# Optimization experiments

Measured on AMD Instinct MI355X. Metric: run time of the kernel, lower is better.

## Reference

```python
import jax, jax.numpy as jnp
from jax import lax
import numpy as np

IMG = 1024                      # image_size (square)
RPN_TRAIN_THRES = 0.5
RATIOS = jnp.array([0.5, 1.0, 2.0], jnp.float32)
SCALES = jnp.array([0.2, 0.4, 0.7], jnp.float32)
K_GT = 16


def _conv(x, w, b, stride):
    # NHWC x HWIO -> NHWC, VALID padding (keras Conv2D default)
    return lax.conv_general_dilated(x, w, (stride, stride), 'VALID',
                                    dimension_numbers=('NHWC', 'HWIO', 'NHWC')) + b


def _anchor_set():
    # [-w/2, -h/2, w/2, h/2] for 9 ratio/scale combos
    rs = jnp.sqrt(RATIOS)[:, None]                      # (3,1)
    ws = (SCALES[None, :] * rs).reshape(-1)             # (9,)
    hs = (SCALES[None, :] / rs).reshape(-1)
    return jnp.stack([ws, hs, ws, hs], axis=1) * 0.5 * jnp.array([-1.0, -1.0, 1.0, 1.0], jnp.float32)


def _anchors_pre(h, w):
    # mirrors generate_anchors_pre (incl. tf.transpose reversing axes -> (W,H,4));
    # feature map is square here so the layout matches the original.
    x = jnp.arange(0.0, 1.0, 1.0 / w, dtype=jnp.float32)
    y = jnp.arange(0.0, 1.0, 1.0 / h, dtype=jnp.float32)
    xx, yy = jnp.meshgrid(x, y)                         # (H,W)
    centers = jnp.stack([xx, yy, xx, yy], 0).transpose(2, 1, 0)  # (W,H,4)
    return centers[:, :, None, :] + _anchor_set()       # (W,H,9,4)


def _iou(b1, b2, gw, gh):
    gwh = jnp.array([gw, gh], jnp.float32)
    s1 = jnp.prod(b1[..., 2:] - b1[..., :2] + gwh, axis=-1)
    s2 = jnp.prod(b2[..., 2:] - b2[..., :2] + gwh, axis=-1)
    xa = jnp.maximum(b1[..., 0], b2[..., 0])
    ya = jnp.maximum(b1[..., 1], b2[..., 1])
    xb = jnp.minimum(b1[..., 2], b2[..., 2])
    yb = jnp.minimum(b1[..., 3], b2[..., 3])
    inter = jnp.maximum(xb - xa + gw, 0.0) * jnp.maximum(yb - ya + gh, 0.0)
    return inter / (s1 + s2 - inter)


def setup_inputs() -> dict:
    key = jax.random.key(0)
    ks = jax.random.split(key, 10)
    image = jax.random.uniform(ks[0], (1, IMG, IMG, 3), jnp.float32)
    cxy = jax.random.uniform(ks[1], (K_GT, 2), jnp.float32, 0.2, 0.8)
    wh = jax.random.uniform(ks[2], (K_GT, 2), jnp.float32, 0.1, 0.4)
    gt_boxes = jnp.concatenate([cxy - wh / 2, cxy + wh / 2], axis=1)  # (K,4) x1,y1,x2,y2
    Wb = jax.random.normal(ks[3], (4, 4, 3, 128), jnp.float32) * 0.05
    bb = jnp.zeros((128,), jnp.float32)
    Wi = jax.random.normal(ks[4], (3, 3, 128, 256), jnp.float32) * 0.05
    bi = jnp.zeros((256,), jnp.float32)
    Wc = jax.random.normal(ks[5], (1, 1, 256, 9), jnp.float32) * 0.05
    bc = jnp.zeros((9,), jnp.float32)
    Wr = jax.random.normal(ks[6], (1, 1, 256, 36), jnp.float32) * 0.05
    br = jnp.zeros((36,), jnp.float32)
    return {'image': image, 'gt_boxes': gt_boxes, 'Wb': Wb, 'bb': bb,
            'Wi': Wi, 'bi': bi, 'Wc': Wc, 'bc': bc, 'Wr': Wr, 'br': br}


def reference(image, gt_boxes, Wb, bb, Wi, bi, Wc, bc, Wr, br):
    feats = _conv(image, Wb, bb, 4)            # backbone: (1,256,256,128)
    fmap = _conv(feats, Wi, bi, 1)             # inter_conv: (1,254,254,256)
    fh, fw = fmap.shape[1], fmap.shape[2]
    gw = 1.0 / IMG
    gh = 1.0 / IMG
    anchors = _anchors_pre(fh, fw).reshape(-1, 4)          # (N,4), N = fh*fw*9
    inside = ((anchors[:, 0] >= 0.0) & (anchors[:, 1] >= 0.0) &
              (anchors[:, 2] < 1.0) & (anchors[:, 3] < 1.0))
    iou = _iou(anchors[:, None, :], gt_boxes[None, :, :], gw, gh)  # (N,K)
    max_iou = jnp.max(iou, axis=1)
    iou_in = jnp.where(inside[:, None], iou, -1.0)
    gt_max_iou = jnp.max(iou_in, axis=0)                   # (K,)
    is_gt_best = jnp.any((iou_in == gt_max_iou[None, :]) & inside[:, None], axis=1)
    pos = inside & (is_gt_best | (max_iou >= RPN_TRAIN_THRES))
    labels = jnp.where(inside, 0.0, -1.0)
    labels = jnp.where(pos, 1.0, labels)                   # (N,) in {-1,0,1}
    # RPN classification loss (BCE with logits) over labels != -1
    cls = _conv(fmap, Wc, bc, 1).reshape(-1)               # (N,)
    sel = (labels != -1.0).astype(jnp.float32)
    lbl = jnp.maximum(labels, 0.0)
    bce = lbl * jax.nn.softplus(-cls) + (1.0 - lbl) * jax.nn.softplus(cls)
    cls_loss = jnp.sum(bce * sel) / jnp.sum(sel)
    # smooth-L1 box loss, faithful to the original (it masks bbox_pred, not the diff)
    reg = _conv(fmap, Wr, br, 1).reshape(-1, 4)            # (N,4)
    m = pos.astype(jnp.float32)[:, None]                   # (N,1) bbox_mask
    ab = jnp.abs(reg * m)
    ss = (ab < 1.0).astype(jnp.float32)
    box_loss = ab * ab * 0.5 * ss + (ab - 0.5) * (1.0 - ss)
    bbox_loss = jnp.sum(box_loss) / jnp.sum(m)
    return cls_loss + bbox_loss
```

## Files before the change

kernel.cpp:

```cpp
#include <hip/hip_runtime.h>

#define F2      254
#define NPIX    (F2 * F2)
#define KGT     16
#define GWC     (1.0f / 1024.0f)

typedef __attribute__((ext_vector_type(8))) short bf16x8;
typedef __attribute__((ext_vector_type(4))) float f32x4;

__device__ unsigned short g_feats[256 * 256 * 128];
__device__ unsigned short g_W2s[36 * 3 * 64 * 8];
__device__ unsigned short g_Wbs[2 * 8 * 64 * 8];
__device__ float          g_b2[48];
__device__ float          g_acc[4] = {0.0f, 0.0f, 0.0f, 0.0f};
__device__ unsigned       g_keys[KGT] = {
    0x407FFFFFu, 0x407FFFFFu, 0x407FFFFFu, 0x407FFFFFu,
    0x407FFFFFu, 0x407FFFFFu, 0x407FFFFFu, 0x407FFFFFu,
    0x407FFFFFu, 0x407FFFFFu, 0x407FFFFFu, 0x407FFFFFu,
    0x407FFFFFu, 0x407FFFFFu, 0x407FFFFFu, 0x407FFFFFu};
__device__ unsigned       g_done = 0u;

__device__ __forceinline__ float b2f(unsigned short h) {
    return __uint_as_float(((unsigned)h) << 16);
}
__device__ __forceinline__ unsigned short f2b(float f) {
    unsigned u = __float_as_uint(f);
    unsigned r = (u + 0x7FFFu + ((u >> 16) & 1u)) >> 16;
    return (unsigned short)r;
}

__device__ __forceinline__ void iou16(float x1, float y1, float x2, float y2,
                                      const float* __restrict__ gt, float* __restrict__ v) {
    float s1 = (x2 - x1 + GWC) * (y2 - y1 + GWC);
#pragma unroll
    for (int k = 0; k < KGT; ++k) {
        float gx1 = gt[k * 4 + 0], gy1 = gt[k * 4 + 1];
        float gx2 = gt[k * 4 + 2], gy2 = gt[k * 4 + 3];
        float s2 = (gx2 - gx1 + GWC) * (gy2 - gy1 + GWC);
        float xa = fmaxf(x1, gx1), ya = fmaxf(y1, gy1);
        float xb = fminf(x2, gx2), yb = fminf(y2, gy2);
        float iw = fmaxf(xb - xa + GWC, 0.0f);
        float ih = fmaxf(yb - ya + GWC, 0.0f);
        float inter = iw * ih;
        v[k] = inter / (s1 + s2 - inter);
    }
}

__device__ __forceinline__ void type_extent(int a, float* hw, float* hh) {
    int ri = a / 3, si = a - ri * 3;
    float rat = (ri == 0) ? 0.5f : (ri == 1) ? 1.0f : 2.0f;
    float scl = (si == 0) ? 0.2f : (si == 1) ? 0.4f : 0.7f;
    float rs = sqrtf(rat);
    *hw = scl * rs * 0.5f;
    *hh = scl / rs * 0.5f;
}

__global__ __launch_bounds__(256) void k_prep(const float* __restrict__ Wi,
                                              const float* __restrict__ bi,
                                              const float* __restrict__ Wc,
                                              const float* __restrict__ bc,
                                              const float* __restrict__ Wr,
                                              const float* __restrict__ br,
                                              const float* __restrict__ Wb,
                                              const float* __restrict__ gt) {
    __shared__ float wcr[256][48];
    __shared__ float red[4][KGT];
    int t = threadIdx.x;
    int b = blockIdx.x;

    if (b >= 292) {
        int bid = b - 292;
        int a = bid >> 5;
        int blk = bid & 31;
        float hw, hh;
        type_extent(a, &hw, &hh);
        float m16[KGT];
#pragma unroll
        for (int k = 0; k < KGT; ++k) m16[k] = -1.0f;
        for (int pix = blk * 256 + t; pix < NPIX; pix += 32 * 256) {
            int w = pix / F2, h = pix - w * F2;
            float cx = (float)w * (1.0f / 254.0f);
            float cy = (float)h * (1.0f / 254.0f);
            float x1 = cx - hw, y1 = cy - hh, x2 = cx + hw, y2 = cy + hh;
            bool inside = (x1 >= 0.0f) && (y1 >= 0.0f) && (x2 < 1.0f) && (y2 < 1.0f);
            if (__ballot(inside) == 0ull) continue;
            if (inside) {
                float v[KGT];
                iou16(x1, y1, x2, y2, gt, v);
#pragma unroll
                for (int k = 0; k < KGT; ++k) m16[k] = fmaxf(m16[k], v[k]);
            }
        }
#pragma unroll
        for (int k = 0; k < KGT; ++k) {
#pragma unroll
            for (int m = 32; m; m >>= 1) m16[k] = fmaxf(m16[k], __shfl_xor(m16[k], m, 64));
        }
        int lane = t & 63, wv = t >> 6;
        if (lane == 0) {
#pragma unroll
            for (int k = 0; k < KGT; ++k) red[wv][k] = m16[k];
        }
        __syncthreads();
        if (t < KGT) {
            float mx = fmaxf(fmaxf(red[0][t], red[1][t]), fmaxf(red[2][t], red[3][t]));
            unsigned u = __float_as_uint(mx);
            unsigned key = (u & 0x80000000u) ? ~u : (u | 0x80000000u);
            atomicMax(&g_keys[t], key);
        }
        return;
    }

    if (b >= 288) {
        int e = (b - 288) * 256 + t;
        int kt = e >> 9, nt = (e >> 6) & 7, l = e & 63;
        unsigned short w8[8];
#pragma unroll
        for (int j = 0; j < 8; ++j) {
            int k = kt * 32 + ((l >> 4) * 8) + j;
            int oc = nt * 16 + (l & 15);
            w8[j] = (k < 48) ? f2b(Wb[(size_t)k * 128 + oc]) : (unsigned short)0;
        }
        *(ulonglong2*)(g_Wbs + (size_t)e * 8) = *(ulonglong2*)w8;
        return;
    }

    for (int i = t; i < 2304; i += 256) wcr[i / 9][i % 9] = Wc[i];
    for (int i = t; i < 9216; i += 256) wcr[i / 36][9 + i % 36] = Wr[i];
    for (int i = t; i < 768; i += 256) wcr[i / 3][45 + i % 3] = 0.0f;
    __syncthreads();

    int wave = __builtin_amdgcn_readfirstlane(t >> 6);
    int lane = t & 63;
    int k = b * 4 + wave;
    int o = min(lane, 47);
    const float* wik = Wi + (size_t)k * 256;
    float acc = 0.0f;
#pragma unroll 8
    for (int oc = 0; oc < 256; ++oc)
        acc = fmaf(wik[oc], wcr[oc][o], acc);

    if (lane < 48) {
        int kt = k >> 5, r5 = k & 31, j = r5 & 7, lhi = r5 >> 3;
        int nt = o >> 4, llo = o & 15, l = lhi * 16 + llo;
        g_W2s[(size_t)((kt * 3 + nt) * 64 + l) * 8 + j] = f2b(acc);
    }
    if (b == 0 && t < 48) {
        float a2 = (t < 9) ? bc[t] : ((t < 45) ? br[t - 9] : 0.0f);
        for (int oc = 0; oc < 256; ++oc) a2 = fmaf(bi[oc], wcr[oc][t], a2);
        g_b2[t] = a2;
    }
}

__device__ __forceinline__ bf16x8 ld_a8(const float* ib, int kbase) {
    int r0 = kbase / 12, q0 = kbase - r0 * 12;
    unsigned short a8[8];
    float4 f0 = *(const float4*)(ib + (size_t)r0 * 3072 + q0);
    int k4 = kbase + 4;
    int r1 = k4 / 12, q1 = k4 - r1 * 12;
    float4 f1 = *(const float4*)(ib + (size_t)r1 * 3072 + q1);
    a8[0] = f2b(f0.x); a8[1] = f2b(f0.y); a8[2] = f2b(f0.z); a8[3] = f2b(f0.w);
    a8[4] = f2b(f1.x); a8[5] = f2b(f1.y); a8[6] = f2b(f1.z); a8[7] = f2b(f1.w);
    return *(bf16x8*)a8;
}

__global__ __launch_bounds__(256) void k_conv1(const float* __restrict__ img,
                                               const float* __restrict__ bb) {
    int t = threadIdx.x;
    int b = blockIdx.x;
    int cid = ((b & 7) << 7) + (b >> 3);
    int l = t & 63;
    int quad = l >> 4;
    int tile = cid * 4 + (t >> 6);
    int m0 = tile * 16;
    int p = m0 + (l & 15);
    int oy = p >> 8, ox = p & 255;
    const float* ib = img + ((size_t)oy * 4 * 1024 + (size_t)ox * 4) * 3;

    bf16x8 a0 = ld_a8(ib, quad * 8);
    bf16x8 a1 = (quad < 2) ? ld_a8(ib, 32 + quad * 8) : (bf16x8){0, 0, 0, 0, 0, 0, 0, 0};

    f32x4 acc[8];
#pragma unroll
    for (int nt = 0; nt < 8; ++nt) acc[nt] = (f32x4){0.0f, 0.0f, 0.0f, 0.0f};
#pragma unroll
    for (int nt = 0; nt < 8; ++nt) {
        bf16x8 b0 = *(const bf16x8*)(g_Wbs + (size_t)(nt * 64 + l) * 8);
        bf16x8 b1 = *(const bf16x8*)(g_Wbs + (size_t)((8 + nt) * 64 + l) * 8);
        acc[nt] = __builtin_amdgcn_mfma_f32_16x16x32_bf16(a0, b0, acc[nt], 0, 0, 0);
        acc[nt] = __builtin_amdgcn_mfma_f32_16x16x32_bf16(a1, b1, acc[nt], 0, 0, 0);
    }

    int n0 = l & 15;
    int mB = m0 + quad * 4;
#pragma unroll
    for (int nt = 0; nt < 8; ++nt) {
        int oc = nt * 16 + n0;
        float bias = bb[oc];
#pragma unroll
        for (int r = 0; r < 4; ++r) {
            g_feats[(size_t)(mB + r) * 128 + oc] = f2b(acc[nt][r] + bias);
        }
    }
}

__global__ __launch_bounds__(256) void k_convC_loss(const float* __restrict__ gt,
                                                    unsigned* __restrict__ out) {
    __shared__ alignas(16) unsigned short Bs[12 * 1536];
    __shared__ float redl[4][4];
    int t = threadIdx.x;
    int b = blockIdx.x;
    int xcd = b & 7;
    int cid = (xcd == 0) ? (b >> 3) : (64 + (xcd - 1) * 63 + (b >> 3));
    int l = t & 63;
    int quad = l >> 4;
    int wv = t >> 6;
    int tile = cid * 4 + wv;
    int m0 = tile * 32;
    int mA0 = min(m0 + (l & 15), NPIX - 1);
    int mA1 = min(m0 + 16 + (l & 15), NPIX - 1);
    int py0 = mA0 / F2, px0 = mA0 - py0 * F2;
    int py1 = mA1 / F2, px1 = mA1 - py1 * F2;

    f32x4 acc[2][3];
#pragma unroll
    for (int h = 0; h < 2; ++h)
#pragma unroll
        for (int nt = 0; nt < 3; ++nt) acc[h][nt] = (f32x4){0.0f, 0.0f, 0.0f, 0.0f};

    for (int c = 0; c < 3; ++c) {
        __syncthreads();
        {
            const uint4* src = (const uint4*)(g_W2s + (size_t)c * 18432);
            uint4* dst = (uint4*)Bs;
#pragma unroll
            for (int j = 0; j < 9; ++j) dst[t + 256 * j] = src[t + 256 * j];
        }
        __syncthreads();
#pragma unroll
        for (int i = 0; i < 12; ++i) {
            int kt = c * 12 + i;
            int pos = kt >> 2, kc = kt & 3;
            int ky = pos / 3, kx = pos - ky * 3;
            const unsigned short* ap0 =
                g_feats + ((size_t)(py0 + ky) * 256 + (px0 + kx)) * 128 + quad * 8 + kc * 32;
            const unsigned short* ap1 =
                g_feats + ((size_t)(py1 + ky) * 256 + (px1 + kx)) * 128 + quad * 8 + kc * 32;
            bf16x8 a0 = *(const bf16x8*)ap0;
            bf16x8 a1 = *(const bf16x8*)ap1;
            const unsigned short* bp = Bs + (size_t)i * 1536 + l * 8;
            bf16x8 b0 = *(const bf16x8*)(bp);
            bf16x8 b1 = *(const bf16x8*)(bp + 512);
            bf16x8 b2v = *(const bf16x8*)(bp + 1024);
            acc[0][0] = __builtin_amdgcn_mfma_f32_16x16x32_bf16(a0, b0, acc[0][0], 0, 0, 0);
            acc[0][1] = __builtin_amdgcn_mfma_f32_16x16x32_bf16(a0, b1, acc[0][1], 0, 0, 0);
            acc[0][2] = __builtin_amdgcn_mfma_f32_16x16x32_bf16(a0, b2v, acc[0][2], 0, 0, 0);
            acc[1][0] = __builtin_amdgcn_mfma_f32_16x16x32_bf16(a1, b0, acc[1][0], 0, 0, 0);
            acc[1][1] = __builtin_amdgcn_mfma_f32_16x16x32_bf16(a1, b1, acc[1][1], 0, 0, 0);
            acc[1][2] = __builtin_amdgcn_mfma_f32_16x16x32_bf16(a1, b2v, acc[1][2], 0, 0, 0);
        }
    }

    __syncthreads();
    float (*S)[129] = (float (*)[129])(void*)Bs;
    int n0 = l & 15;
#pragma unroll
    for (int h = 0; h < 2; ++h) {
        int plB = wv * 32 + h * 16 + quad * 4;
#pragma unroll
        for (int nt = 0; nt < 3; ++nt) {
            int n = nt * 16 + n0;
            float bias = g_b2[n];
#pragma unroll
            for (int r = 0; r < 4; ++r) S[n][plB + r] = acc[h][nt][r] + bias;
        }
    }
    __syncthreads();

    int m0b = cid * 128;
    float sb = 0.0f, ss = 0.0f, sx = 0.0f, sp = 0.0f;
    for (int idx = t; idx < 1152; idx += 256) {
        int a = idx >> 7;
        int pl = idx & 127;
        int m = m0b + pl;
        float hw, hhf;
        type_extent(a, &hw, &hhf);
        bool inside = false;
        float x1 = 0.0f, y1 = 0.0f, x2 = 0.0f, y2 = 0.0f;
        if (m < NPIX) {
            int pw = m / F2, ph = m - pw * F2;
            float cx = (float)pw * (1.0f / 254.0f);
            float cy = (float)ph * (1.0f / 254.0f);
            x1 = cx - hw; y1 = cy - hhf; x2 = cx + hw; y2 = cy + hhf;
            inside = (x1 >= 0.0f) && (y1 >= 0.0f) && (x2 < 1.0f) && (y2 < 1.0f);
        }
        if (__ballot(inside) == 0ull) continue;
        if (inside) {
            float v[KGT];
            iou16(x1, y1, x2, y2, gt, v);
            float maxi = -1.0f;
            bool best = false;
#pragma unroll
            for (int k = 0; k < KGT; ++k) {
                maxi = fmaxf(maxi, v[k]);
                unsigned e = g_keys[k];
                float gm = __uint_as_float((e & 0x80000000u) ? (e & 0x7FFFFFFFu) : ~e);
                best = best || (v[k] == gm);
            }
            bool ispos = best || (maxi >= 0.5f);
            float c = b2f(f2b(S[a][pl]));
            float z = ispos ? -c : c;
            sb += fmaxf(z, 0.0f) + log1pf(expf(-fabsf(z)));
            ss += 1.0f;
            if (ispos) {
                float aa;
                aa = fabsf(b2f(f2b(S[9 + 4 * a + 0][pl]))); sx += (aa < 1.0f) ? 0.5f * aa * aa : aa - 0.5f;
                aa = fabsf(b2f(f2b(S[9 + 4 * a + 1][pl]))); sx += (aa < 1.0f) ? 0.5f * aa * aa : aa - 0.5f;
                aa = fabsf(b2f(f2b(S[9 + 4 * a + 2][pl]))); sx += (aa < 1.0f) ? 0.5f * aa * aa : aa - 0.5f;
                aa = fabsf(b2f(f2b(S[9 + 4 * a + 3][pl]))); sx += (aa < 1.0f) ? 0.5f * aa * aa : aa - 0.5f;
                sp += 1.0f;
            }
        }
    }

#pragma unroll
    for (int mm = 32; mm; mm >>= 1) {
        sb += __shfl_xor(sb, mm, 64);
        ss += __shfl_xor(ss, mm, 64);
        sx += __shfl_xor(sx, mm, 64);
        sp += __shfl_xor(sp, mm, 64);
    }
    int lane = t & 63;
    if (lane == 0) { redl[wv][0] = sb; redl[wv][1] = ss; redl[wv][2] = sx; redl[wv][3] = sp; }
    __syncthreads();
    if (t < 4) {
        float s = redl[0][t] + redl[1][t] + redl[2][t] + redl[3][t];
        atomicAdd(&g_acc[t], s);
    }
    __syncthreads();
    if (t == 0) {
        unsigned prev = atomicAdd(&g_done, 1u);
        if (prev == 504u) {
            float a0 = atomicAdd(&g_acc[0], 0.0f);
            float a1 = atomicAdd(&g_acc[1], 0.0f);
            float a2 = atomicAdd(&g_acc[2], 0.0f);
            float a3 = atomicAdd(&g_acc[3], 0.0f);
            float res = a0 / a1 + a2 / a3;
            unsigned lo = (unsigned)f2b(res);
            unsigned hi = __float_as_uint(res) >> 16;
            out[0] = (hi << 16) | lo;
            g_acc[0] = 0.0f; g_acc[1] = 0.0f; g_acc[2] = 0.0f; g_acc[3] = 0.0f;
#pragma unroll
            for (int k = 0; k < KGT; ++k) g_keys[k] = 0x407FFFFFu;
            g_done = 0u;
        }
    }
}

extern "C" void kernel_launch(void* const* d_in, const int* in_sizes, int n_in,
                              void* d_out, int out_size, void* d_ws, size_t ws_size,
                              hipStream_t stream) {
    (void)in_sizes; (void)n_in; (void)out_size; (void)d_ws; (void)ws_size;
    const float* image = (const float*)d_in[0];
    const float* gt    = (const float*)d_in[1];
    const float* Wb    = (const float*)d_in[2];
    const float* bb    = (const float*)d_in[3];
    const float* Wi    = (const float*)d_in[4];
    const float* bi    = (const float*)d_in[5];
    const float* Wc    = (const float*)d_in[6];
    const float* bc    = (const float*)d_in[7];
    const float* Wr    = (const float*)d_in[8];
    const float* br    = (const float*)d_in[9];

    k_prep      <<<580, 256, 0, stream>>>(Wi, bi, Wc, bc, Wr, br, Wb, gt);
    k_conv1     <<<1024, 256, 0, stream>>>(image, bb);
    k_convC_loss<<<505, 256, 0, stream>>>(gt, (unsigned*)d_out);
}
```

Before: 132.4 us.

## Merge prep and conv1 kernels into one launch with per-block weight staging

Fuses the weight-prep/anchor-IoU kernel and the first conv kernel into a single 1600-block launch. Each conv1 block now converts the Wb weights to bf16 in shared memory itself instead of reading a global buffer written by a prior kernel, which removes a kernel boundary and launch gap. The folded-weight computation is split into two passes over a half-size shared buffer to fit the shared union. Costs are redundant Wb conversion in every conv block and more shared memory per block, which may reduce occupancy.

```diff
diff --git a/kernel.cpp b/kernel.cpp
--- a/kernel.cpp
+++ b/kernel.cpp
@@ -10,7 +10,6 @@
 
 __device__ unsigned short g_feats[256 * 256 * 128];
 __device__ unsigned short g_W2s[36 * 3 * 64 * 8];
-__device__ unsigned short g_Wbs[2 * 8 * 64 * 8];
 __device__ float          g_b2[48];
 __device__ float          g_acc[4] = {0.0f, 0.0f, 0.0f, 0.0f};
 __device__ unsigned       g_keys[KGT] = {
@@ -55,21 +54,133 @@
     *hh = scl / rs * 0.5f;
 }
 
-__global__ __launch_bounds__(256) void k_prep(const float* __restrict__ Wi,
-                                              const float* __restrict__ bi,
-                                              const float* __restrict__ Wc,
-                                              const float* __restrict__ bc,
-                                              const float* __restrict__ Wr,
-                                              const float* __restrict__ br,
-                                              const float* __restrict__ Wb,
-                                              const float* __restrict__ gt) {
-    __shared__ float wcr[256][48];
+__device__ __forceinline__ bf16x8 ld_a8(const float* ib, int kbase) {
+    int r0 = kbase / 12, q0 = kbase - r0 * 12;
+    unsigned short a8[8];
+    float4 f0 = *(const float4*)(ib + (size_t)r0 * 3072 + q0);
+    int k4 = kbase + 4;
+    int r1 = k4 / 12, q1 = k4 - r1 * 12;
+    float4 f1 = *(const float4*)(ib + (size_t)r1 * 3072 + q1);
+    a8[0] = f2b(f0.x); a8[1] = f2b(f0.y); a8[2] = f2b(f0.z); a8[3] = f2b(f0.w);
+    a8[4] = f2b(f1.x); a8[5] = f2b(f1.y); a8[6] = f2b(f1.z); a8[7] = f2b(f1.w);
+    return *(bf16x8*)a8;
+}
+
+__global__ __launch_bounds__(256) void k_front(const float* __restrict__ img,
+                                               const float* __restrict__ bb,
+                                               const float* __restrict__ Wb,
+                                               const float* __restrict__ Wi,
+                                               const float* __restrict__ bi,
+                                               const float* __restrict__ Wc,
+                                               const float* __restrict__ bc,
+                                               const float* __restrict__ Wr,
+                                               const float* __restrict__ br,
+                                               const float* __restrict__ gt) {
+    __shared__ alignas(16) char sbuf[128 * 48 * 4];
     __shared__ float red[4][KGT];
     int t = threadIdx.x;
     int b = blockIdx.x;
 
-    if (b >= 292) {
-        int bid = b - 292;
+    if (b < 1024) {
+        unsigned short* wbs = (unsigned short*)sbuf;
+#pragma unroll
+        for (int it = 0; it < 4; ++it) {
+            int e = t + it * 256;
+            int kt = e >> 9, nt = (e >> 6) & 7, l = e & 63;
+            unsigned short w8[8];
+#pragma unroll
+            for (int j = 0; j < 8; ++j) {
+                int k = kt * 32 + ((l >> 4) * 8) + j;
+                int oc = nt * 16 + (l & 15);
+                w8[j] = (k < 48) ? f2b(Wb[(size_t)k * 128 + oc]) : (unsigned short)0;
+            }
+            *(ulonglong2*)(wbs + (size_t)e * 8) = *(ulonglong2*)w8;
+        }
+        __syncthreads();
+
+        int cid = ((b & 7) << 7) + (b >> 3);
+        int l = t & 63;
+        int quad = l >> 4;
+        int tile = cid * 4 + (t >> 6);
+        int m0 = tile * 16;
+        int p = m0 + (l & 15);
+        int oy = p >> 8, ox = p & 255;
+        const float* ib = img + ((size_t)oy * 4 * 1024 + (size_t)ox * 4) * 3;
+
+        bf16x8 a0 = ld_a8(ib, quad * 8);
+        bf16x8 a1 = (quad < 2) ? ld_a8(ib, 32 + quad * 8) : (bf16x8){0, 0, 0, 0, 0, 0, 0, 0};
+
+        f32x4 acc[8];
+#pragma unroll
+        for (int nt = 0; nt < 8; ++nt) acc[nt] = (f32x4){0.0f, 0.0f, 0.0f, 0.0f};
+#pragma unroll
+        for (int nt = 0; nt < 8; ++nt) {
+            bf16x8 b0 = *(const bf16x8*)(wbs + (size_t)(nt * 64 + l) * 8);
+            bf16x8 b1 = *(const bf16x8*)(wbs + (size_t)((8 + nt) * 64 + l) * 8);
+            acc[nt] = __builtin_amdgcn_mfma_f32_16x16x32_bf16(a0, b0, acc[nt], 0, 0, 0);
+            acc[nt] = __builtin_amdgcn_mfma_f32_16x16x32_bf16(a1, b1, acc[nt], 0, 0, 0);
+        }
+
+        int n0 = l & 15;
+        int mB = m0 + quad * 4;
+#pragma unroll
+        for (int nt = 0; nt < 8; ++nt) {
+            int oc = nt * 16 + n0;
+            float bias = bb[oc];
+#pragma unroll
+            for (int r = 0; r < 4; ++r) {
+                g_feats[(size_t)(mB + r) * 128 + oc] = f2b(acc[nt][r] + bias);
+            }
+        }
+        return;
+    }
+
+    if (b < 1312) {
+        float (*wcr2)[48] = (float (*)[48])sbuf;
+        int bw = b - 1024;
+        int wave = __builtin_amdgcn_readfirstlane(t >> 6);
+        int lane = t & 63;
+        int k = bw * 4 + wave;
+        int o = min(lane, 47);
+        const float* wik = Wi + (size_t)k * 256;
+        float acc = 0.0f;
+        bool bias_thr = (b == 1024) && (t < 48);
+        float a2 = 0.0f;
+        if (bias_thr) a2 = (t < 9) ? bc[t] : ((t < 45) ? br[t - 9] : 0.0f);
+
+        for (int pss = 0; pss < 2; ++pss) {
+            __syncthreads();
+            int ocb = pss * 128;
+            for (int i = t; i < 1152; i += 256) {
+                int oc = i / 9;
+                wcr2[oc][i % 9] = Wc[(size_t)(ocb + oc) * 9 + i % 9];
+            }
+            for (int i = t; i < 4608; i += 256) {
+                int oc = i / 36;
+                wcr2[oc][9 + i % 36] = Wr[(size_t)(ocb + oc) * 36 + i % 36];
+            }
+            for (int i = t; i < 384; i += 256) wcr2[i / 3][45 + i % 3] = 0.0f;
+            __syncthreads();
+#pragma unroll 8
+            for (int oc = 0; oc < 128; ++oc)
+                acc = fmaf(wik[ocb + oc], wcr2[oc][o], acc);
+            if (bias_thr) {
+                for (int oc = 0; oc < 128; ++oc)
+                    a2 = fmaf(bi[ocb + oc], wcr2[oc][t], a2);
+            }
+        }
+
+        if (lane < 48) {
+            int kt = k >> 5, r5 = k & 31, j = r5 & 7, lhi = r5 >> 3;
+            int nt = o >> 4, llo = o & 15, l2 = lhi * 16 + llo;
+            g_W2s[(size_t)((kt * 3 + nt) * 64 + l2) * 8 + j] = f2b(acc);
+        }
+        if (bias_thr) g_b2[t] = a2;
+        return;
+    }
+
+    {
+        int bid = b - 1312;
         int a = bid >> 5;
         int blk = bid & 31;
         float hw, hh;
@@ -107,99 +218,6 @@
             unsigned u = __float_as_uint(mx);
             unsigned key = (u & 0x80000000u) ? ~u : (u | 0x80000000u);
             atomicMax(&g_keys[t], key);
-        }
-        return;
-    }
-
-    if (b >= 288) {
-        int e = (b - 288) * 256 + t;
-        int kt = e >> 9, nt = (e >> 6) & 7, l = e & 63;
-        unsigned short w8[8];
-#pragma unroll
-        for (int j = 0; j < 8; ++j) {
-            int k = kt * 32 + ((l >> 4) * 8) + j;
-            int oc = nt * 16 + (l & 15);
-            w8[j] = (k < 48) ? f2b(Wb[(size_t)k * 128 + oc]) : (unsigned short)0;
-        }
-        *(ulonglong2*)(g_Wbs + (size_t)e * 8) = *(ulonglong2*)w8;
-        return;
-    }
-
-    for (int i = t; i < 2304; i += 256) wcr[i / 9][i % 9] = Wc[i];
-    for (int i = t; i < 9216; i += 256) wcr[i / 36][9 + i % 36] = Wr[i];
-    for (int i = t; i < 768; i += 256) wcr[i / 3][45 + i % 3] = 0.0f;
-    __syncthreads();
-
-    int wave = __builtin_amdgcn_readfirstlane(t >> 6);
-    int lane = t & 63;
-    int k = b * 4 + wave;
-    int o = min(lane, 47);
-    const float* wik = Wi + (size_t)k * 256;
-    float acc = 0.0f;
-#pragma unroll 8
-    for (int oc = 0; oc < 256; ++oc)
-        acc = fmaf(wik[oc], wcr[oc][o], acc);
-
-    if (lane < 48) {
-        int kt = k >> 5, r5 = k & 31, j = r5 & 7, lhi = r5 >> 3;
-        int nt = o >> 4, llo = o & 15, l = lhi * 16 + llo;
-        g_W2s[(size_t)((kt * 3 + nt) * 64 + l) * 8 + j] = f2b(acc);
-    }
-    if (b == 0 && t < 48) {
-        float a2 = (t < 9) ? bc[t] : ((t < 45) ? br[t - 9] : 0.0f);
-        for (int oc = 0; oc < 256; ++oc) a2 = fmaf(bi[oc], wcr[oc][t], a2);
-        g_b2[t] = a2;
-    }
-}
-
-__device__ __forceinline__ bf16x8 ld_a8(const float* ib, int kbase) {
-    int r0 = kbase / 12, q0 = kbase - r0 * 12;
-    unsigned short a8[8];
-    float4 f0 = *(const float4*)(ib + (size_t)r0 * 3072 + q0);
-    int k4 = kbase + 4;
-    int r1 = k4 / 12, q1 = k4 - r1 * 12;
-    float4 f1 = *(const float4*)(ib + (size_t)r1 * 3072 + q1);
-    a8[0] = f2b(f0.x); a8[1] = f2b(f0.y); a8[2] = f2b(f0.z); a8[3] = f2b(f0.w);
-    a8[4] = f2b(f1.x); a8[5] = f2b(f1.y); a8[6] = f2b(f1.z); a8[7] = f2b(f1.w);
-    return *(bf16x8*)a8;
-}
-
-__global__ __launch_bounds__(256) void k_conv1(const float* __restrict__ img,
-                                               const float* __restrict__ bb) {
-    int t = threadIdx.x;
-    int b = blockIdx.x;
-    int cid = ((b & 7) << 7) + (b >> 3);
-    int l = t & 63;
-    int quad = l >> 4;
-    int tile = cid * 4 + (t >> 6);
-    int m0 = tile * 16;
-    int p = m0 + (l & 15);
-    int oy = p >> 8, ox = p & 255;
-    const float* ib = img + ((size_t)oy * 4 * 1024 + (size_t)ox * 4) * 3;
-
-    bf16x8 a0 = ld_a8(ib, quad * 8);
-    bf16x8 a1 = (quad < 2) ? ld_a8(ib, 32 + quad * 8) : (bf16x8){0, 0, 0, 0, 0, 0, 0, 0};
-
-    f32x4 acc[8];
-#pragma unroll
-    for (int nt = 0; nt < 8; ++nt) acc[nt] = (f32x4){0.0f, 0.0f, 0.0f, 0.0f};
-#pragma unroll
-    for (int nt = 0; nt < 8; ++nt) {
-        bf16x8 b0 = *(const bf16x8*)(g_Wbs + (size_t)(nt * 64 + l) * 8);
-        bf16x8 b1 = *(const bf16x8*)(g_Wbs + (size_t)((8 + nt) * 64 + l) * 8);
-        acc[nt] = __builtin_amdgcn_mfma_f32_16x16x32_bf16(a0, b0, acc[nt], 0, 0, 0);
-        acc[nt] = __builtin_amdgcn_mfma_f32_16x16x32_bf16(a1, b1, acc[nt], 0, 0, 0);
-    }
-
-    int n0 = l & 15;
-    int mB = m0 + quad * 4;
-#pragma unroll
-    for (int nt = 0; nt < 8; ++nt) {
-        int oc = nt * 16 + n0;
-        float bias = bb[oc];
-#pragma unroll
-        for (int r = 0; r < 4; ++r) {
-            g_feats[(size_t)(mB + r) * 128 + oc] = f2b(acc[nt][r] + bias);
         }
     }
 }
@@ -372,7 +390,6 @@
     const float* Wr    = (const float*)d_in[8];
     const float* br    = (const float*)d_in[9];
 
-    k_prep      <<<580, 256, 0, stream>>>(Wi, bi, Wc, bc, Wr, br, Wb, gt);
-    k_conv1     <<<1024, 256, 0, stream>>>(image, bb);
+    k_front     <<<1600, 256, 0, stream>>>(image, bb, Wb, Wi, bi, Wc, bc, Wr, br, gt);
     k_convC_loss<<<505, 256, 0, stream>>>(gt, (unsigned*)d_out);
 }
```

After: 125.7 us. 5.1% less time.
